# Kernel tuning notes

Measured on AMD Instinct MI355X. Metric: run time of the kernel, lower is better.

## Reference

```python
import jax, jax.numpy as jnp
import numpy as np

B, S, D, M = 8, 128, 512, 4
DEPTH, THR, TEMP, EPS = 16, 0.9999, 1.0, 1e-6


def setup_inputs() -> dict:
    key = jax.random.key(0)
    ks = jax.random.split(key, 13)
    def nrm(k, shape):
        return jax.random.normal(k, shape, jnp.float32) / np.sqrt(shape[-1]).astype(np.float32)
    return dict(
        x_real=jax.random.normal(ks[0], (B, S, D), jnp.float32),
        x_imag=jax.random.normal(ks[1], (B, S, D), jnp.float32),
        Wq_r=nrm(ks[2], (M, D, D)), Wq_i=nrm(ks[3], (M, D, D)),
        Wk_r=nrm(ks[4], (M, D, D)), Wk_i=nrm(ks[5], (M, D, D)),
        Wv_r=nrm(ks[6], (M, D, D)), Wv_i=nrm(ks[7], (M, D, D)),
        mod_bias=jnp.zeros((M, D), jnp.float32),
        ln_scale=jnp.ones((M, D), jnp.float32),
        ln_shift=jnp.zeros((M, D), jnp.float32),
        w_sal=nrm(ks[8], (M, 2 * D)),
        gru_Wih=nrm(ks[9], (2 * D, 3 * D)),
        gru_Whh=nrm(ks[10], (D, 3 * D)),
        gru_bih=jnp.zeros((3 * D,), jnp.float32),
        gru_bhh=jnp.zeros((3 * D,), jnp.float32),
        bias_W=nrm(ks[11], (D, M)),
        bias_b=jnp.zeros((M,), jnp.float32),
        w_halt=nrm(ks[12], (2 * D,)),
        b_halt=jnp.zeros((1,), jnp.float32),
    )


def reference(x_real, x_imag, Wq_r, Wq_i, Wk_r, Wk_i, Wv_r, Wv_i,
              mod_bias, ln_scale, ln_shift, w_sal,
              gru_Wih, gru_Whh, gru_bih, gru_bhh,
              bias_W, bias_b, w_halt, b_halt):
    scale = D ** -0.5

    def clin(xr, xi, Wr, Wi):
        # ComplexLinear broadcast over module axis: x [B,S,D], W [M,D,D] -> [M,B,S,D]
        rr = jnp.einsum('bsd,mde->mbse', xr, Wr)
        ii = jnp.einsum('bsd,mde->mbse', xi, Wi)
        ri = jnp.einsum('bsd,mde->mbse', xr, Wi)
        ir = jnp.einsum('bsd,mde->mbse', xi, Wr)
        return rr - ii, ri + ir

    def modules(zr, zi):
        # all M processor modules in parallel: ComplexAttention -> ModReLU -> ComplexLayerNorm
        qr, qi = clin(zr, zi, Wq_r, Wq_i)
        kr, ki = clin(zr, zi, Wk_r, Wk_i)
        vr, vi = clin(zr, zi, Wv_r, Wv_i)
        qf = jnp.concatenate([qr, qi], -1)            # [M,B,S,2D]
        kf = jnp.concatenate([kr, ki], -1)
        attn = jax.nn.softmax(jnp.einsum('mbsd,mbtd->mbst', qf, kf) * scale, -1)
        or_ = jnp.einsum('mbst,mbtd->mbsd', attn, vr)
        oi_ = jnp.einsum('mbst,mbtd->mbsd', attn, vi)
        # ModReLU
        mag = jnp.sqrt(or_ ** 2 + oi_ ** 2) + EPS
        g = jax.nn.relu(mag + mod_bias[:, None, None, :]) / mag
        or_, oi_ = or_ * g, oi_ * g
        # ComplexLayerNorm (normalize magnitude, keep phase; torch var is unbiased)
        mag = jnp.sqrt(or_ ** 2 + oi_ ** 2) + EPS
        mu = mag.mean(-1, keepdims=True)
        var = jnp.var(mag, axis=-1, keepdims=True, ddof=1)
        nm = (mag - mu) / jnp.sqrt(var + EPS)
        nm = nm * ln_scale[:, None, None, :] + ln_shift[:, None, None, :]
        ph = jnp.arctan2(oi_, or_)
        return nm * jnp.cos(ph), nm * jnp.sin(ph)

    def gru(xf, h):
        gx = xf @ gru_Wih + gru_bih
        gh = h @ gru_Whh + gru_bhh
        xr_, xz_, xn_ = jnp.split(gx, 3, -1)
        hr_, hz_, hn_ = jnp.split(gh, 3, -1)
        r = jax.nn.sigmoid(xr_ + hr_)
        zg = jax.nn.sigmoid(xz_ + hz_)
        n = jnp.tanh(xn_ + r * hn_)
        return (1.0 - zg) * n + zg * h

    def step(carry, _):
        zr, zi, h, cum, ar, ai, pond = carry
        pooled = jnp.concatenate([zr.mean(1), zi.mean(1)], -1)   # [B,2D]
        h = gru(pooled, h)                                       # ExecutiveController
        mbias = h @ bias_W + bias_b                              # [B,M]
        mr, mi = modules(zr, zi)                                 # [M,B,S,D]
        feat = jnp.concatenate([mr.mean(2), mi.mean(2)], -1)     # [M,B,2D]
        sal = jnp.einsum('mbf,mf->mb', feat, w_sal)              # salience
        w = jax.nn.softmax((sal + mbias.T) / TEMP, axis=0)       # module competition
        gr = jnp.einsum('mb,mbsd->bsd', w, mr)                   # global workspace broadcast
        gi = jnp.einsum('mb,mbsd->bsd', w, mi)
        gwp = jnp.concatenate([gr.mean(1), gi.mean(1)], -1)
        p = jax.nn.sigmoid(gwp @ w_halt + b_halt[0])             # [B] halting prob
        still = (cum < THR).astype(p.dtype)
        new_halt = ((cum + p) >= THR) & (cum < THR)
        wt = jnp.where(new_halt, 1.0 - cum, p) * still           # ACT weights
        cum = cum + wt
        ar = ar + wt[:, None, None] * gr
        ai = ai + wt[:, None, None] * gi
        pond = pond + still
        return (gr, gi, h, cum, ar, ai, pond), None

    z0 = jnp.zeros((B,), x_real.dtype)
    init = (x_real, x_imag, jnp.zeros((B, D), x_real.dtype), z0,
            jnp.zeros_like(x_real), jnp.zeros_like(x_imag), z0)
    (zr, zi, h, cum, ar, ai, pond), _ = jax.lax.scan(step, init, None, length=DEPTH)
    return jnp.stack([ar, ai])  # [2,B,S,D] accumulated workspace (real, imag)
```

## Files before the change

kernel.cpp:

```cpp
#include <hip/hip_runtime.h>
#include <math.h>

#define B 8
#define S 128
#define D 512
#define M 4
#define BS 1024
#define BSD 524288
#define DEPTH 16
#define THRESH 0.9999f
#define EPS 1e-6f
#define SCALE 0.04419417382415922f

typedef float floatx4 __attribute__((ext_vector_type(4)));
typedef short s8v __attribute__((ext_vector_type(8)));
typedef unsigned short us4 __attribute__((ext_vector_type(4)));

__device__ __forceinline__ unsigned short f2bf(float f) {
  unsigned int u = __float_as_uint(f);
  u += 0x7FFFu + ((u >> 16) & 1u);
  return (unsigned short)(u >> 16);
}
__device__ __forceinline__ float bf2f(unsigned short h) {
  return __uint_as_float((unsigned int)h << 16);
}

__device__ __forceinline__ void gll16(const void* g, void* l) {
  __builtin_amdgcn_global_load_lds(
      (const __attribute__((address_space(1))) unsigned int*)g,
      (__attribute__((address_space(3))) unsigned int*)l, 16, 0, 0);
}

#define OFF_ZR   0
#define OFF_ZI   (1*BSD)
#define OFF_AR   (2*BSD)
#define OFF_AI   (3*BSD)
#define OFF_OR   (4*BSD)
#define OFF_OI   (8*BSD)
#define OFF_FEAT (12*BSD)
#define OFF_GWP  (12*BSD + 65536)
#define OFF_H0   (12*BSD + 73728)
#define OFF_H1   (12*BSD + 77824)
#define OFF_CUM  (12*BSD + 81920)
#define OFF_W    (12*BSD + 81928)
#define OFF_WT   (12*BSD + 81960)
#define OFF_CUM2 (12*BSD + 81968)
#define OFF_PART OFF_ZR
#define OFF_XH   (12*BSD + 90112)
#define OFF_XL   (OFF_XH + 1*BSD)
#define OFF_WH   (OFF_XH + 2*BSD)
#define OFF_WL   (OFF_XH + 8*BSD)
#define OFF_QCH  (OFF_XH + 14*BSD)
#define OFF_QCL  (OFF_XH + 18*BSD)
#define OFF_KCH  (OFF_XH + 22*BSD)
#define OFF_KCL  (OFF_XH + 26*BSD)
#define OFF_VTH  (OFF_XH + 30*BSD)
#define OFF_VTL  (OFF_XH + 34*BSD)
#define OFF_PH   (OFF_XH + 38*BSD)
#define OFF_PL   (OFF_PH + 262144)

__global__ __launch_bounds__(256) void k_init(const float* __restrict__ xr,
                                              const float* __restrict__ xi,
                                              float* __restrict__ ws) {
  unsigned short* xh = (unsigned short*)(ws + OFF_XH);
  unsigned short* xl = (unsigned short*)(ws + OFF_XL);
  int i4 = blockIdx.x * 256 + threadIdx.x;
  float4 a = ((const float4*)xr)[i4];
  float4 b = ((const float4*)xi)[i4];
  ((float4*)(ws + OFF_ZR))[i4] = a;
  ((float4*)(ws + OFF_ZI))[i4] = b;
  float4 z = {0.f, 0.f, 0.f, 0.f};
  ((float4*)(ws + OFF_AR))[i4] = z;
  ((float4*)(ws + OFF_AI))[i4] = z;
  int row = i4 >> 7;
  int d4 = (i4 & 127) * 4;
  float av[4] = {a.x, a.y, a.z, a.w}, bv[4] = {b.x, b.y, b.z, b.w};
  us4 hh, hl;
#pragma unroll
  for (int j = 0; j < 4; ++j) {
    unsigned short h = f2bf(av[j]); hh[j] = h; hl[j] = f2bf(av[j] - bf2f(h));
  }
  *(us4*)(xh + (size_t)row * 1024 + d4) = hh;
  *(us4*)(xl + (size_t)row * 1024 + d4) = hl;
#pragma unroll
  for (int j = 0; j < 4; ++j) {
    unsigned short h = f2bf(bv[j]); hh[j] = h; hl[j] = f2bf(bv[j] - bf2f(h));
  }
  *(us4*)(xh + (size_t)row * 1024 + 512 + d4) = hh;
  *(us4*)(xl + (size_t)row * 1024 + 512 + d4) = hl;
  if (i4 < (B * D) / 4) {
    ((float4*)(ws + OFF_H0))[i4] = z;
    ((float4*)(ws + OFF_H1))[i4] = z;
  }
  if (i4 < 16384) ((float4*)(ws + OFF_FEAT))[i4] = z;
  if (i4 < 2048)  ((float4*)(ws + OFF_GWP))[i4] = z;
  if (i4 < B) { ws[OFF_CUM + i4] = 0.f; ws[OFF_CUM2 + i4] = 0.f; }
}

__global__ __launch_bounds__(256) void k_wprep(const float* __restrict__ Wqr,
                                               const float* __restrict__ Wqi,
                                               const float* __restrict__ Wkr,
                                               const float* __restrict__ Wki,
                                               const float* __restrict__ Wvr,
                                               const float* __restrict__ Wvi,
                                               float* __restrict__ ws) {
  __shared__ float lt[64][65];
  unsigned short* wh = (unsigned short*)(ws + OFF_WH);
  unsigned short* wl = (unsigned short*)(ws + OFF_WL);
  int z = blockIdx.z, m = z / 6, idx = z % 6;
  const float* Wsrc;
  switch (idx) {
    case 0:  Wsrc = Wqr; break;
    case 1:  Wsrc = Wqi; break;
    case 2:  Wsrc = Wkr; break;
    case 3:  Wsrc = Wki; break;
    case 4:  Wsrc = Wvr; break;
    default: Wsrc = Wvi; break;
  }
  Wsrc += (size_t)m * D * D;
  int k0 = blockIdx.x * 64, n0 = blockIdx.y * 64;
  int tx = threadIdx.x & 63, ty = threadIdx.x >> 6;
#pragma unroll
  for (int i = 0; i < 16; ++i) {
    int kl = ty + i * 4;
    lt[kl][tx] = Wsrc[(size_t)(k0 + kl) * D + n0 + tx];
  }
  __syncthreads();
  unsigned short* whp = wh + (size_t)z * 262144;
  unsigned short* wlp = wl + (size_t)z * 262144;
#pragma unroll
  for (int i = 0; i < 16; ++i) {
    int nl = ty + i * 4;
    float v = lt[tx][nl];
    unsigned short h = f2bf(v);
    whp[(size_t)(n0 + nl) * 512 + k0 + tx] = h;
    wlp[(size_t)(n0 + nl) * 512 + k0 + tx] = f2bf(v - bf2f(h));
  }
}

__global__ __launch_bounds__(256) void k_gwp(const float* __restrict__ zr,
                                             const float* __restrict__ zi,
                                             float* __restrict__ gwp) {
  int idx = blockIdx.x * 256 + threadIdx.x;
  int b = idx >> 10;
  int f = idx & 1023;
  const float* src = (f < D) ? (zr + b * S * D + f) : (zi + b * S * D + (f - D));
  float s = 0.f;
#pragma unroll 8
  for (int ss = 0; ss < S; ++ss) s += src[ss * D];
  gwp[idx] = s * (1.0f / S);
}

__global__ __launch_bounds__(256) void k_qk(float* __restrict__ ws) {
  __shared__ __align__(16) unsigned short Ah[128 * 32], Al[128 * 32];
  __shared__ __align__(16) unsigned short Bh[128 * 32], Bl[128 * 32];
  int t = threadIdx.x;
  if (blockIdx.x == 0 && blockIdx.y == 0 && blockIdx.z == 0) {
    float4 z4 = {0.f, 0.f, 0.f, 0.f};
    for (int i = t; i < 4096; i += 256) ((float4*)(ws + OFF_PART))[i] = z4;
  }
  const unsigned short* xh = (const unsigned short*)(ws + OFF_XH);
  const unsigned short* xl = (const unsigned short*)(ws + OFF_XL);
  const unsigned short* wh = (const unsigned short*)(ws + OFF_WH);
  const unsigned short* wl = (const unsigned short*)(ws + OFF_WL);
  int z = blockIdx.z, m = z >> 2, w6 = z & 3;
  int pair = (w6 >> 1) * 2;
  int p1 = m * 6 + pair + (w6 & 1);
  int p2 = m * 6 + pair + ((w6 & 1) ^ 1);
  bool neg2 = ((w6 & 1) == 0);
  const unsigned short* PH1 = wh + (size_t)p1 * 262144;
  const unsigned short* PL1 = wl + (size_t)p1 * 262144;
  const unsigned short* PH2 = wh + (size_t)p2 * 262144;
  const unsigned short* PL2 = wl + (size_t)p2 * 262144;

  int row0 = blockIdx.y * 128;
  int col0 = blockIdx.x * 128;
  int lane = t & 63, w = t >> 6;
  int wr = w >> 1, wc = w & 1;
  int q = lane >> 4, r = lane & 15;
  int srow = t >> 2;
  int skoff = (t & 3) * 8;
  size_t wrow1 = (size_t)(col0 + srow) * 512 + skoff;
  size_t wrow2 = (size_t)(col0 + 64 + srow) * 512 + skoff;
  size_t xrow1 = (size_t)(row0 + srow) * 1024 + skoff;
  size_t xrow2 = (size_t)(row0 + 64 + srow) * 1024 + skoff;
  const s8v sgn = {(short)0x8000, (short)0x8000, (short)0x8000, (short)0x8000,
                   (short)0x8000, (short)0x8000, (short)0x8000, (short)0x8000};

  floatx4 acc[4][4];
#pragma unroll
  for (int i = 0; i < 4; ++i)
#pragma unroll
    for (int j = 0; j < 4; ++j) acc[i][j] = (floatx4){0.f, 0.f, 0.f, 0.f};

  for (int k0 = 0; k0 < 1024; k0 += 32) {
    const unsigned short *WgH, *WgL;
    int kk = k0;
    bool xon = false;
    if (k0 < 512) { WgH = PH1; WgL = PL1; }
    else          { WgH = PH2; WgL = PL2; kk = k0 - 512; xon = neg2; }
    gll16(xh + xrow1 + k0, (char*)Ah + t * 16);
    gll16(xh + xrow2 + k0, (char*)Ah + 4096 + t * 16);
    gll16(xl + xrow1 + k0, (char*)Al + t * 16);
    gll16(xl + xrow2 + k0, (char*)Al + 4096 + t * 16);
    gll16(WgH + wrow1 + kk, (char*)Bh + t * 16);
    gll16(WgH + wrow2 + kk, (char*)Bh + 4096 + t * 16);
    gll16(WgL + wrow1 + kk, (char*)Bl + t * 16);
    gll16(WgL + wrow2 + kk, (char*)Bl + 4096 + t * 16);
    __syncthreads();
    s8v ah[4], al[4], bh[4], bl[4];
#pragma unroll
    for (int i = 0; i < 4; ++i) {
      int ro = (wr * 64 + i * 16 + r) * 32 + q * 8;
      ah[i] = *(const s8v*)((const short*)Ah + ro);
      al[i] = *(const s8v*)((const short*)Al + ro);
    }
#pragma unroll
    for (int j = 0; j < 4; ++j) {
      int ro = (wc * 64 + j * 16 + r) * 32 + q * 8;
      bh[j] = *(const s8v*)((const short*)Bh + ro);
      bl[j] = *(const s8v*)((const short*)Bl + ro);
    }
    if (xon) {
#pragma unroll
      for (int j = 0; j < 4; ++j) { bh[j] = bh[j] ^ sgn; bl[j] = bl[j] ^ sgn; }
    }
#pragma unroll
    for (int i = 0; i < 4; ++i)
#pragma unroll
      for (int j = 0; j < 4; ++j) {
        acc[i][j] = __builtin_amdgcn_mfma_f32_16x16x32_bf16(ah[i], bh[j], acc[i][j], 0, 0, 0);
        acc[i][j] = __builtin_amdgcn_mfma_f32_16x16x32_bf16(ah[i], bl[j], acc[i][j], 0, 0, 0);
        acc[i][j] = __builtin_amdgcn_mfma_f32_16x16x32_bf16(al[i], bh[j], acc[i][j], 0, 0, 0);
      }
    __syncthreads();
  }
  unsigned short *dh, *dl;
  if (w6 < 2) { dh = (unsigned short*)(ws + OFF_QCH); dl = (unsigned short*)(ws + OFF_QCL); }
  else        { dh = (unsigned short*)(ws + OFF_KCH); dl = (unsigned short*)(ws + OFF_KCL); }
  int half = (w6 & 1) * 512;
  size_t base = (size_t)m * 1024 * 1024;
#pragma unroll
  for (int i = 0; i < 4; ++i)
#pragma unroll
    for (int j = 0; j < 4; ++j) {
      int rowb = row0 + wr * 64 + i * 16 + q * 4;
      int colb = col0 + wc * 64 + j * 16 + r;
#pragma unroll
      for (int reg = 0; reg < 4; ++reg) {
        float v = acc[i][j][reg];
        unsigned short h = f2bf(v);
        size_t idx = base + (size_t)(rowb + reg) * 1024 + half + colb;
        dh[idx] = h;
        dl[idx] = f2bf(v - bf2f(h));
      }
    }
}

__global__ __launch_bounds__(256) void k_vattn(float* __restrict__ ws,
                                               const float* __restrict__ gwp,
                                               const float* __restrict__ hold,
                                               const float* __restrict__ Wih,
                                               const float* __restrict__ Whh) {
  __shared__ __align__(16) unsigned short Ah[128 * 32], Al[128 * 32];
  __shared__ __align__(16) unsigned short Bh[128 * 32], Bl[128 * 32];
  __shared__ float rmax[64][4];
  __shared__ float rsum[64][4];
  int t = threadIdx.x;
  int blk = blockIdx.x;

  if (blk >= 320) {
    float* xbuf = (float*)Ah;
    float* hbuf = (float*)Al;
    float (*red)[64][4] = (float (*)[64][4])Bh;
    int idx = blk - 320;
    int b = idx >> 5;
    int cc = (idx >> 2) & 7;
    int kq = idx & 3;
    int c0 = cc * 64;
    int td = t & 63, ks = t >> 6;
    for (int f = t; f < 1024; f += 256) xbuf[f] = gwp[b * 1024 + f];
    for (int d2 = t; d2 < 512; d2 += 256) hbuf[d2] = hold[b * 512 + d2];
    __syncthreads();
    float aR = 0.f, aZ = 0.f, aXn = 0.f, aHn = 0.f;
    int kbeg = kq * 384 + ks * 96, kend = kbeg + 96;
#pragma unroll 8
    for (int kk = kbeg; kk < kend; ++kk) {
      bool ih = kk < 1024;
      float x = ih ? xbuf[kk] : hbuf[kk - 1024];
      const float* base = ih ? (Wih + (size_t)kk * 1536) : (Whh + (size_t)(kk - 1024) * 1536);
      float wr = base[c0 + td];
      float wz = base[512 + c0 + td];
      float wn = base[1024 + c0 + td];
      aR += x * wr;
      aZ += x * wz;
      if (ih) aXn += x * wn; else aHn += x * wn;
    }
    red[ks][td][0] = aR;
    red[ks][td][1] = aZ;
    red[ks][td][2] = aXn;
    red[ks][td][3] = aHn;
    __syncthreads();
    if (t < 64) {
      float r_ = 0.f, z_ = 0.f, xn = 0.f, hn = 0.f;
#pragma unroll
      for (int s = 0; s < 4; ++s) {
        r_ += red[s][t][0]; z_ += red[s][t][1]; xn += red[s][t][2]; hn += red[s][t][3];
      }
      float* part = ws + OFF_PART + ((size_t)b * 512 + c0 + t) * 4;
      atomicAdd(part + 0, r_);
      atomicAdd(part + 1, z_);
      atomicAdd(part + 2, xn);
      atomicAdd(part + 3, hn);
    }
    return;
  }

  if (blk >= 256) {
    const unsigned short* qch = (const unsigned short*)(ws + OFF_QCH);
    const unsigned short* qcl = (const unsigned short*)(ws + OFF_QCL);
    const unsigned short* kch = (const unsigned short*)(ws + OFF_KCH);
    const unsigned short* kcl = (const unsigned short*)(ws + OFF_KCL);
    unsigned short* ph = (unsigned short*)(ws + OFF_PH);
    unsigned short* pl = (unsigned short*)(ws + OFF_PL);
    int ablk = blk - 256, mb = ablk >> 1, half = ablk & 1;
    size_t gbase = (size_t)mb * 128 * 1024;
    int lane = t & 63, wc = t >> 6;
    int q = lane >> 4, r = lane & 15;
    int srow = t >> 2;
    int skoff = (t & 3) * 8;
    size_t arow = gbase + (size_t)(half * 64 + srow) * 1024 + skoff;
    size_t brow1 = gbase + (size_t)srow * 1024 + skoff;
    size_t brow2 = gbase + (size_t)(64 + srow) * 1024 + skoff;

    floatx4 acc[4][2];
#pragma unroll
    for (int i = 0; i < 4; ++i)
#pragma unroll
      for (int j = 0; j < 2; ++j) acc[i][j] = (floatx4){0.f, 0.f, 0.f, 0.f};

    for (int k0 = 0; k0 < 1024; k0 += 32) {
      gll16(qch + arow + k0, (char*)Ah + t * 16);
      gll16(qcl + arow + k0, (char*)Al + t * 16);
      gll16(kch + brow1 + k0, (char*)Bh + t * 16);
      gll16(kch + brow2 + k0, (char*)Bh + 4096 + t * 16);
      gll16(kcl + brow1 + k0, (char*)Bl + t * 16);
      gll16(kcl + brow2 + k0, (char*)Bl + 4096 + t * 16);
      __syncthreads();
      s8v ah[4], al[4], bh[2], bl[2];
#pragma unroll
      for (int i = 0; i < 4; ++i) {
        int ro = (i * 16 + r) * 32 + q * 8;
        ah[i] = *(const s8v*)((const short*)Ah + ro);
        al[i] = *(const s8v*)((const short*)Al + ro);
      }
#pragma unroll
      for (int j = 0; j < 2; ++j) {
        int ro = (wc * 32 + j * 16 + r) * 32 + q * 8;
        bh[j] = *(const s8v*)((const short*)Bh + ro);
        bl[j] = *(const s8v*)((const short*)Bl + ro);
      }
#pragma unroll
      for (int i = 0; i < 4; ++i)
#pragma unroll
        for (int j = 0; j < 2; ++j) {
          acc[i][j] = __builtin_amdgcn_mfma_f32_16x16x32_bf16(ah[i], bh[j], acc[i][j], 0, 0, 0);
          acc[i][j] = __builtin_amdgcn_mfma_f32_16x16x32_bf16(ah[i], bl[j], acc[i][j], 0, 0, 0);
          acc[i][j] = __builtin_amdgcn_mfma_f32_16x16x32_bf16(al[i], bh[j], acc[i][j], 0, 0, 0);
        }
      __syncthreads();
    }
#pragma unroll
    for (int i = 0; i < 4; ++i)
#pragma unroll
      for (int j = 0; j < 2; ++j)
#pragma unroll
        for (int reg = 0; reg < 4; ++reg) acc[i][j][reg] *= SCALE;
#pragma unroll
    for (int i = 0; i < 4; ++i)
#pragma unroll
      for (int reg = 0; reg < 4; ++reg) {
        float mx = fmaxf(acc[i][0][reg], acc[i][1][reg]);
        for (int o = 1; o < 16; o <<= 1) mx = fmaxf(mx, __shfl_xor(mx, o));
        if (r == 0) rmax[i * 16 + q * 4 + reg][wc] = mx;
      }
    __syncthreads();
#pragma unroll
    for (int i = 0; i < 4; ++i)
#pragma unroll
      for (int reg = 0; reg < 4; ++reg) {
        int row = i * 16 + q * 4 + reg;
        float gmx = fmaxf(fmaxf(rmax[row][0], rmax[row][1]),
                          fmaxf(rmax[row][2], rmax[row][3]));
        float sm = 0.f;
#pragma unroll
        for (int j = 0; j < 2; ++j) {
          float e = __expf(acc[i][j][reg] - gmx);
          acc[i][j][reg] = e;
          sm += e;
        }
        for (int o = 1; o < 16; o <<= 1) sm += __shfl_xor(sm, o);
        if (r == 0) rsum[row][wc] = sm;
      }
    __syncthreads();
#pragma unroll
    for (int i = 0; i < 4; ++i)
#pragma unroll
      for (int reg = 0; reg < 4; ++reg) {
        int row = i * 16 + q * 4 + reg;
        float inv = 1.f / (rsum[row][0] + rsum[row][1] + rsum[row][2] + rsum[row][3]);
        size_t rb = (size_t)(mb * 128 + half * 64 + row) * 128;
#pragma unroll
        for (int j = 0; j < 2; ++j) {
          float p = acc[i][j][reg] * inv;
          unsigned short h = f2bf(p);
          size_t idx = rb + wc * 32 + j * 16 + r;
          ph[idx] = h;
          pl[idx] = f2bf(p - bf2f(h));
        }
      }
    return;
  }

  const unsigned short* xh = (const unsigned short*)(ws + OFF_XH);
  const unsigned short* xl = (const unsigned short*)(ws + OFF_XL);
  const unsigned short* wh = (const unsigned short*)(ws + OFF_WH);
  const unsigned short* wl = (const unsigned short*)(ws + OFF_WL);
  int plane = blk >> 5, m = plane >> 1, w6 = 4 + (plane & 1);
  int bx = (blk & 31) >> 3, by = blk & 7;
  int p1 = m * 6 + 4 + (w6 & 1);
  int p2 = m * 6 + 4 + ((w6 & 1) ^ 1);
  bool neg2 = ((w6 & 1) == 0);
  const unsigned short* PH1 = wh + (size_t)p1 * 262144;
  const unsigned short* PL1 = wl + (size_t)p1 * 262144;
  const unsigned short* PH2 = wh + (size_t)p2 * 262144;
  const unsigned short* PL2 = wl + (size_t)p2 * 262144;

  int row0 = bx * 128;
  int col0 = by * 128;
  int lane = t & 63, w = t >> 6;
  int wr = w >> 1, wc = w & 1;
  int q = lane >> 4, r = lane & 15;
  int srow = t >> 2;
  int skoff = (t & 3) * 8;
  size_t wrow1 = (size_t)(row0 + srow) * 512 + skoff;
  size_t wrow2 = (size_t)(row0 + 64 + srow) * 512 + skoff;
  size_t xrow1 = (size_t)(col0 + srow) * 1024 + skoff;
  size_t xrow2 = (size_t)(col0 + 64 + srow) * 1024 + skoff;
  const s8v sgn = {(short)0x8000, (short)0x8000, (short)0x8000, (short)0x8000,
                   (short)0x8000, (short)0x8000, (short)0x8000, (short)0x8000};

  floatx4 acc[4][4];
#pragma unroll
  for (int i = 0; i < 4; ++i)
#pragma unroll
    for (int j = 0; j < 4; ++j) acc[i][j] = (floatx4){0.f, 0.f, 0.f, 0.f};

  for (int k0 = 0; k0 < 1024; k0 += 32) {
    const unsigned short *WgH, *WgL;
    int kk = k0;
    bool xon = false;
    if (k0 < 512) { WgH = PH1; WgL = PL1; }
    else          { WgH = PH2; WgL = PL2; kk = k0 - 512; xon = neg2; }
    gll16(WgH + wrow1 + kk, (char*)Ah + t * 16);
    gll16(WgH + wrow2 + kk, (char*)Ah + 4096 + t * 16);
    gll16(WgL + wrow1 + kk, (char*)Al + t * 16);
    gll16(WgL + wrow2 + kk, (char*)Al + 4096 + t * 16);
    gll16(xh + xrow1 + k0, (char*)Bh + t * 16);
    gll16(xh + xrow2 + k0, (char*)Bh + 4096 + t * 16);
    gll16(xl + xrow1 + k0, (char*)Bl + t * 16);
    gll16(xl + xrow2 + k0, (char*)Bl + 4096 + t * 16);
    __syncthreads();
    s8v ah[4], al[4], bh[4], bl[4];
#pragma unroll
    for (int i = 0; i < 4; ++i) {
      int ro = (wr * 64 + i * 16 + r) * 32 + q * 8;
      ah[i] = *(const s8v*)((const short*)Ah + ro);
      al[i] = *(const s8v*)((const short*)Al + ro);
    }
#pragma unroll
    for (int j = 0; j < 4; ++j) {
      int ro = (wc * 64 + j * 16 + r) * 32 + q * 8;
      bh[j] = *(const s8v*)((const short*)Bh + ro);
      bl[j] = *(const s8v*)((const short*)Bl + ro);
    }
    if (xon) {
#pragma unroll
      for (int i = 0; i < 4; ++i) { ah[i] = ah[i] ^ sgn; al[i] = al[i] ^ sgn; }
    }
#pragma unroll
    for (int i = 0; i < 4; ++i)
#pragma unroll
      for (int j = 0; j < 4; ++j) {
        acc[i][j] = __builtin_amdgcn_mfma_f32_16x16x32_bf16(ah[i], bh[j], acc[i][j], 0, 0, 0);
        acc[i][j] = __builtin_amdgcn_mfma_f32_16x16x32_bf16(ah[i], bl[j], acc[i][j], 0, 0, 0);
        acc[i][j] = __builtin_amdgcn_mfma_f32_16x16x32_bf16(al[i], bh[j], acc[i][j], 0, 0, 0);
      }
    __syncthreads();
  }
  unsigned short* dh = (unsigned short*)(ws + OFF_VTH);
  unsigned short* dl = (unsigned short*)(ws + OFF_VTL);
  size_t base = (size_t)((w6 & 1) * 4 + m) * 512 * 1024;
#pragma unroll
  for (int i = 0; i < 4; ++i)
#pragma unroll
    for (int j = 0; j < 4; ++j) {
      int rowb = row0 + wr * 64 + i * 16 + q * 4;
      int colb = col0 + wc * 64 + j * 16 + r;
#pragma unroll
      for (int reg = 0; reg < 4; ++reg) {
        float v = acc[i][j][reg];
        unsigned short h = f2bf(v);
        size_t idx = base + (size_t)(rowb + reg) * 1024 + colb;
        dh[idx] = h;
        dl[idx] = f2bf(v - bf2f(h));
      }
    }
}

__global__ __launch_bounds__(256) void k_pv(float* __restrict__ ws) {
  __shared__ __align__(16) unsigned short Ph_[128 * 32], Pl_[128 * 32];
  __shared__ __align__(16) unsigned short VrH[128 * 32], VrL[128 * 32];
  __shared__ __align__(16) unsigned short ViH[128 * 32], ViL[128 * 32];
  const unsigned short* ph = (const unsigned short*)(ws + OFF_PH);
  const unsigned short* pl = (const unsigned short*)(ws + OFF_PL);
  const unsigned short* vth = (const unsigned short*)(ws + OFF_VTH);
  const unsigned short* vtl = (const unsigned short*)(ws + OFF_VTL);
  int mb = blockIdx.y, m = mb >> 3, b = mb & 7;
  int col0 = blockIdx.x * 128;
  int t = threadIdx.x, lane = t & 63, w = t >> 6;
  int wr = w >> 1, wc = w & 1;
  int q = lane >> 4, r = lane & 15;
  int srow = t >> 2;
  int skoff = (t & 3) * 8;
  size_t prow1 = (size_t)(mb * 128 + srow) * 128 + skoff;
  size_t prow2 = (size_t)(mb * 128 + 64 + srow) * 128 + skoff;
  size_t vbr1 = ((size_t)(m * 512) + col0 + srow) * 1024 + b * 128 + skoff;
  size_t vbr2 = ((size_t)(m * 512) + col0 + 64 + srow) * 1024 + b * 128 + skoff;
  size_t vplane_i = (size_t)4 * 512 * 1024;

  floatx4 accR[4][4], accI[4][4];
#pragma unroll
  for (int i = 0; i < 4; ++i)
#pragma unroll
    for (int j = 0; j < 4; ++j) {
      accR[i][j] = (floatx4){0.f, 0.f, 0.f, 0.f};
      accI[i][j] = (floatx4){0.f, 0.f, 0.f, 0.f};
    }

  for (int k0 = 0; k0 < 128; k0 += 32) {
    gll16(ph + prow1 + k0, (char*)Ph_ + t * 16);
    gll16(ph + prow2 + k0, (char*)Ph_ + 4096 + t * 16);
    gll16(pl + prow1 + k0, (char*)Pl_ + t * 16);
    gll16(pl + prow2 + k0, (char*)Pl_ + 4096 + t * 16);
    gll16(vth + vbr1 + k0, (char*)VrH + t * 16);
    gll16(vth + vbr2 + k0, (char*)VrH + 4096 + t * 16);
    gll16(vtl + vbr1 + k0, (char*)VrL + t * 16);
    gll16(vtl + vbr2 + k0, (char*)VrL + 4096 + t * 16);
    gll16(vth + vplane_i + vbr1 + k0, (char*)ViH + t * 16);
    gll16(vth + vplane_i + vbr2 + k0, (char*)ViH + 4096 + t * 16);
    gll16(vtl + vplane_i + vbr1 + k0, (char*)ViL + t * 16);
    gll16(vtl + vplane_i + vbr2 + k0, (char*)ViL + 4096 + t * 16);
    __syncthreads();
    s8v ah[4], al[4];
#pragma unroll
    for (int i = 0; i < 4; ++i) {
      int ro = (wr * 64 + i * 16 + r) * 32 + q * 8;
      ah[i] = *(const s8v*)((const short*)Ph_ + ro);
      al[i] = *(const s8v*)((const short*)Pl_ + ro);
    }
#pragma unroll
    for (int j = 0; j < 4; ++j) {
      int ro = (wc * 64 + j * 16 + r) * 32 + q * 8;
      s8v vrh = *(const s8v*)((const short*)VrH + ro);
      s8v vrl = *(const s8v*)((const short*)VrL + ro);
      s8v vih = *(const s8v*)((const short*)ViH + ro);
      s8v vil = *(const s8v*)((const short*)ViL + ro);
#pragma unroll
      for (int i = 0; i < 4; ++i) {
        accR[i][j] = __builtin_amdgcn_mfma_f32_16x16x32_bf16(ah[i], vrh, accR[i][j], 0, 0, 0);
        accR[i][j] = __builtin_amdgcn_mfma_f32_16x16x32_bf16(ah[i], vrl, accR[i][j], 0, 0, 0);
        accR[i][j] = __builtin_amdgcn_mfma_f32_16x16x32_bf16(al[i], vrh, accR[i][j], 0, 0, 0);
        accI[i][j] = __builtin_amdgcn_mfma_f32_16x16x32_bf16(ah[i], vih, accI[i][j], 0, 0, 0);
        accI[i][j] = __builtin_amdgcn_mfma_f32_16x16x32_bf16(ah[i], vil, accI[i][j], 0, 0, 0);
        accI[i][j] = __builtin_amdgcn_mfma_f32_16x16x32_bf16(al[i], vih, accI[i][j], 0, 0, 0);
      }
    }
    __syncthreads();
  }
  float* orp = ws + OFF_OR + (size_t)mb * 128 * 512;
  float* oip = ws + OFF_OI + (size_t)mb * 128 * 512;
#pragma unroll
  for (int i = 0; i < 4; ++i)
#pragma unroll
    for (int j = 0; j < 4; ++j) {
      int rowb = wr * 64 + i * 16 + q * 4;
      int colb = col0 + wc * 64 + j * 16 + r;
#pragma unroll
      for (int reg = 0; reg < 4; ++reg) {
        orp[(size_t)(rowb + reg) * 512 + colb] = accR[i][j][reg];
        oip[(size_t)(rowb + reg) * 512 + colb] = accI[i][j][reg];
      }
    }
}

__global__ __launch_bounds__(256) void k_modlnfeat(float* __restrict__ ws,
                                                   const float* __restrict__ mod_bias,
                                                   const float* __restrict__ ln_scale,
                                                   const float* __restrict__ ln_shift,
                                                   const float* __restrict__ hold,
                                                   float* __restrict__ hnew,
                                                   const float* __restrict__ bih,
                                                   const float* __restrict__ bhh) {
  int blk = blockIdx.x;
  int t = threadIdx.x;
  if (blk >= 128) {
    int b = blk - 128;
    for (int c = t; c < 512; c += 256) {
      const float* part = ws + OFF_PART + ((size_t)b * 512 + c) * 4;
      float r_ = part[0] + bih[c] + bhh[c];
      float z_ = part[1] + bih[512 + c] + bhh[512 + c];
      float xn = part[2] + bih[1024 + c];
      float hn = part[3] + bhh[1024 + c];
      float r = 1.f / (1.f + expf(-r_));
      float z = 1.f / (1.f + expf(-z_));
      float n = tanhf(xn + r * hn);
      hnew[b * 512 + c] = (1.f - z) * n + z * hold[b * 512 + c];
    }
    return;
  }
  int mb = blk >> 2, grp = blk & 3;
  int m = mb >> 3;
  int w = t >> 6, l = t & 63;
  int e0 = l * 8;
  float mb_[8], lsc[8], lsh[8];
  *(float4*)&mb_[0] = *(const float4*)(mod_bias + m * 512 + e0);
  *(float4*)&mb_[4] = *(const float4*)(mod_bias + m * 512 + e0 + 4);
  *(float4*)&lsc[0] = *(const float4*)(ln_scale + m * 512 + e0);
  *(float4*)&lsc[4] = *(const float4*)(ln_scale + m * 512 + e0 + 4);
  *(float4*)&lsh[0] = *(const float4*)(ln_shift + m * 512 + e0);
  *(float4*)&lsh[4] = *(const float4*)(ln_shift + m * 512 + e0 + 4);
  float featR[8] = {}, featI[8] = {};
  for (int it = 0; it < 8; ++it) {
    int s = grp * 32 + it * 4 + w;
    float* orp = ws + OFF_OR + ((size_t)mb * 128 + s) * 512 + e0;
    float* oip = ws + OFF_OI + ((size_t)mb * 128 + s) * 512 + e0;
    float orv[8], oiv[8], magv[8];
    *(float4*)&orv[0] = *(const float4*)orp;
    *(float4*)&orv[4] = *(const float4*)(orp + 4);
    *(float4*)&oiv[0] = *(const float4*)oip;
    *(float4*)&oiv[4] = *(const float4*)(oip + 4);
    float sum = 0.f, sumsq = 0.f;
#pragma unroll
    for (int j = 0; j < 8; ++j) {
      float o_r = orv[j], o_i = oiv[j];
      float mag = sqrtf(o_r * o_r + o_i * o_i) + EPS;
      float g = fmaxf(mag + mb_[j], 0.f) / mag;
      o_r *= g; o_i *= g;
      orv[j] = o_r; oiv[j] = o_i;
      float mag2 = sqrtf(o_r * o_r + o_i * o_i) + EPS;
      magv[j] = mag2;
      sum += mag2;
      sumsq += mag2 * mag2;
    }
    for (int o = 1; o < 64; o <<= 1) {
      sum += __shfl_xor(sum, o);
      sumsq += __shfl_xor(sumsq, o);
    }
    float mu = sum * (1.f / D);
    float var = (sumsq - (float)D * mu * mu) * (1.f / (D - 1));
    float inv = 1.f / sqrtf(var + EPS);
#pragma unroll
    for (int j = 0; j < 8; ++j) {
      float nm = (magv[j] - mu) * inv * lsc[j] + lsh[j];
      float hyp = magv[j] - EPS;
      float cp, sp;
      if (hyp > 0.f) { cp = orv[j] / hyp; sp = oiv[j] / hyp; }
      else           { cp = 1.f;          sp = 0.f; }
      orv[j] = nm * cp;
      oiv[j] = nm * sp;
      featR[j] += orv[j];
      featI[j] += oiv[j];
    }
    *(float4*)orp = *(float4*)&orv[0];
    *(float4*)(orp + 4) = *(float4*)&orv[4];
    *(float4*)oip = *(float4*)&oiv[0];
    *(float4*)(oip + 4) = *(float4*)&oiv[4];
  }
  float* fb = ws + OFF_FEAT + (size_t)mb * 1024;
#pragma unroll
  for (int j = 0; j < 8; ++j) {
    atomicAdd(fb + e0 + j, featR[j] * (1.0f / S));
    atomicAdd(fb + 512 + e0 + j, featI[j] * (1.0f / S));
  }
}

__global__ __launch_bounds__(256) void k_wsel(float* __restrict__ ws,
                                              const float* __restrict__ hnew,
                                              const float* __restrict__ bias_W,
                                              const float* __restrict__ bias_b,
                                              const float* __restrict__ w_sal) {
  __shared__ float mb_s[B][M];
  __shared__ float sal_s[M][B];
  int t = threadIdx.x;
  int p = t >> 3, l = t & 7;
  {
    int b = p >> 2, m = p & 3;
    float s = 0.f;
    for (int d2 = l; d2 < D; d2 += 8) s += hnew[b * D + d2] * bias_W[d2 * M + m];
    for (int o = 1; o < 8; o <<= 1) s += __shfl_xor(s, o);
    if (l == 0) mb_s[b][m] = s + bias_b[m];
  }
  {
    int m = p >> 3, b = p & 7;
    float s = 0.f;
    for (int f = l; f < 2 * D; f += 8) s += ws[OFF_FEAT + (m * B + b) * 2 * D + f] * w_sal[m * 2 * D + f];
    for (int o = 1; o < 8; o <<= 1) s += __shfl_xor(s, o);
    if (l == 0) sal_s[m][b] = s;
  }
  __syncthreads();
  if (t < B) {
    int b = t;
    float lg[M], mx = -1e30f;
#pragma unroll
    for (int m = 0; m < M; ++m) { lg[m] = sal_s[m][b] + mb_s[b][m]; mx = fmaxf(mx, lg[m]); }
    float sm = 0.f;
#pragma unroll
    for (int m = 0; m < M; ++m) { lg[m] = expf(lg[m] - mx); sm += lg[m]; }
    float inv = 1.f / sm;
#pragma unroll
    for (int m = 0; m < M; ++m) ws[OFF_W + m * B + b] = lg[m] * inv;
  }
  float4 z4 = {0.f, 0.f, 0.f, 0.f};
  for (int i = t; i < 16384; i += 256) ((float4*)(ws + OFF_FEAT))[i] = z4;
  for (int i = t; i < 2048; i += 256) ((float4*)(ws + OFF_GWP))[i] = z4;
}

__global__ __launch_bounds__(256) void k_bcast(float* __restrict__ ws) {
  __shared__ float pr[1024];
  unsigned short* xh = (unsigned short*)(ws + OFF_XH);
  unsigned short* xl = (unsigned short*)(ws + OFF_XL);
  int t = threadIdx.x;
  int i4 = blockIdx.x * 256 + t;
  int b = i4 >> 14;
  int l = t & 127;
  float w0 = ws[OFF_W + 0 * B + b], w1 = ws[OFF_W + 1 * B + b];
  float w2 = ws[OFF_W + 2 * B + b], w3 = ws[OFF_W + 3 * B + b];
  const float4* mr = (const float4*)(ws + OFF_OR);
  const float4* mi = (const float4*)(ws + OFF_OI);
  const int MS = BSD / 4;
  int row = i4 >> 7;
  int d4 = (i4 & 127) * 4;
  float4 r0 = mr[i4], r1 = mr[i4 + MS], r2 = mr[i4 + 2 * MS], r3 = mr[i4 + 3 * MS];
  float gvR[4];
  gvR[0] = w0 * r0.x + w1 * r1.x + w2 * r2.x + w3 * r3.x;
  gvR[1] = w0 * r0.y + w1 * r1.y + w2 * r2.y + w3 * r3.y;
  gvR[2] = w0 * r0.z + w1 * r1.z + w2 * r2.z + w3 * r3.z;
  gvR[3] = w0 * r0.w + w1 * r1.w + w2 * r2.w + w3 * r3.w;
  ((float4*)(ws + OFF_ZR))[i4] = (float4){gvR[0], gvR[1], gvR[2], gvR[3]};
  us4 hh, hl;
#pragma unroll
  for (int j = 0; j < 4; ++j) {
    unsigned short h = f2bf(gvR[j]); hh[j] = h; hl[j] = f2bf(gvR[j] - bf2f(h));
  }
  *(us4*)(xh + (size_t)row * 1024 + d4) = hh;
  *(us4*)(xl + (size_t)row * 1024 + d4) = hl;
  float4 s0 = mi[i4], s1 = mi[i4 + MS], s2 = mi[i4 + 2 * MS], s3 = mi[i4 + 3 * MS];
  float gvI[4];
  gvI[0] = w0 * s0.x + w1 * s1.x + w2 * s2.x + w3 * s3.x;
  gvI[1] = w0 * s0.y + w1 * s1.y + w2 * s2.y + w3 * s3.y;
  gvI[2] = w0 * s0.z + w1 * s1.z + w2 * s2.z + w3 * s3.z;
  gvI[3] = w0 * s0.w + w1 * s1.w + w2 * s2.w + w3 * s3.w;
  ((float4*)(ws + OFF_ZI))[i4] = (float4){gvI[0], gvI[1], gvI[2], gvI[3]};
#pragma unroll
  for (int j = 0; j < 4; ++j) {
    unsigned short h = f2bf(gvI[j]); hh[j] = h; hl[j] = f2bf(gvI[j] - bf2f(h));
  }
  *(us4*)(xh + (size_t)row * 1024 + 512 + d4) = hh;
  *(us4*)(xl + (size_t)row * 1024 + 512 + d4) = hl;
  if (t < 128) {
#pragma unroll
    for (int j = 0; j < 4; ++j) { pr[l * 4 + j] = gvR[j]; pr[512 + l * 4 + j] = gvI[j]; }
  }
  __syncthreads();
  if (t >= 128) {
#pragma unroll
    for (int j = 0; j < 4; ++j) { pr[l * 4 + j] += gvR[j]; pr[512 + l * 4 + j] += gvI[j]; }
  }
  __syncthreads();
  for (int pp = t; pp < 1024; pp += 256)
    atomicAdd(ws + OFF_GWP + b * 1024 + pp, pr[pp] * (1.0f / S));
}

__global__ __launch_bounds__(256) void k_acchalt(float* __restrict__ ws,
                                                 const float* __restrict__ w_halt,
                                                 const float* __restrict__ b_halt,
                                                 const float* __restrict__ cumr,
                                                 float* __restrict__ cumw) {
  __shared__ float sred[4];
  int t = threadIdx.x;
  int i4 = blockIdx.x * 256 + t;
  int b = i4 >> 14;
  float4 g = *(const float4*)(ws + OFF_GWP + b * 1024 + t * 4);
  float4 wv = *(const float4*)(w_halt + t * 4);
  float s = g.x * wv.x + g.y * wv.y + g.z * wv.z + g.w * wv.w;
  for (int o = 1; o < 64; o <<= 1) s += __shfl_xor(s, o);
  if ((t & 63) == 0) sred[t >> 6] = s;
  __syncthreads();
  float tot = sred[0] + sred[1] + sred[2] + sred[3];
  float p = 1.f / (1.f + expf(-(tot + b_halt[0])));
  float cum = cumr[b];
  float still = (cum < THRESH) ? 1.f : 0.f;
  bool nh = ((cum + p) >= THRESH) && (cum < THRESH);
  float wt = (nh ? (1.f - cum) : p) * still;
  if (((blockIdx.x & 63) == 0) && t == 0) cumw[b] = cum + wt;
  float4 z = ((const float4*)(ws + OFF_ZR))[i4];
  float4 a = ((float4*)(ws + OFF_AR))[i4];
  a.x += wt * z.x; a.y += wt * z.y; a.z += wt * z.z; a.w += wt * z.w;
  ((float4*)(ws + OFF_AR))[i4] = a;
  z = ((const float4*)(ws + OFF_ZI))[i4];
  a = ((float4*)(ws + OFF_AI))[i4];
  a.x += wt * z.x; a.y += wt * z.y; a.z += wt * z.z; a.w += wt * z.w;
  ((float4*)(ws + OFF_AI))[i4] = a;
}

__global__ __launch_bounds__(256) void k_out(const float* __restrict__ ws,
                                             float* __restrict__ out) {
  int i4 = blockIdx.x * 256 + threadIdx.x;
  ((float4*)out)[i4] = ((const float4*)(ws + OFF_AR))[i4];
  ((float4*)out)[i4 + BSD / 4] = ((const float4*)(ws + OFF_AI))[i4];
}

extern "C" void kernel_launch(void* const* d_in, const int* in_sizes, int n_in,
                              void* d_out, int out_size, void* d_ws, size_t ws_size,
                              hipStream_t stream) {
  (void)in_sizes; (void)n_in; (void)out_size; (void)ws_size;
  const float* x_real  = (const float*)d_in[0];
  const float* x_imag  = (const float*)d_in[1];
  const float* Wq_r    = (const float*)d_in[2];
  const float* Wq_i    = (const float*)d_in[3];
  const float* Wk_r    = (const float*)d_in[4];
  const float* Wk_i    = (const float*)d_in[5];
  const float* Wv_r    = (const float*)d_in[6];
  const float* Wv_i    = (const float*)d_in[7];
  const float* mod_bias = (const float*)d_in[8];
  const float* ln_scale = (const float*)d_in[9];
  const float* ln_shift = (const float*)d_in[10];
  const float* w_sal   = (const float*)d_in[11];
  const float* gru_Wih = (const float*)d_in[12];
  const float* gru_Whh = (const float*)d_in[13];
  const float* gru_bih = (const float*)d_in[14];
  const float* gru_bhh = (const float*)d_in[15];
  const float* bias_W  = (const float*)d_in[16];
  const float* bias_b  = (const float*)d_in[17];
  const float* w_halt  = (const float*)d_in[18];
  const float* b_halt  = (const float*)d_in[19];
  float* ws = (float*)d_ws;
  float* out = (float*)d_out;

  k_wprep<<<dim3(8, 8, 24), 256, 0, stream>>>(Wq_r, Wq_i, Wk_r, Wk_i, Wv_r, Wv_i, ws);
  k_init<<<512, 256, 0, stream>>>(x_real, x_imag, ws);
  k_gwp<<<32, 256, 0, stream>>>(ws + OFF_ZR, ws + OFF_ZI, ws + OFF_GWP);
  for (int step = 0; step < DEPTH; ++step) {
    const float* hold = ws + ((step & 1) ? OFF_H1 : OFF_H0);
    float* hnew = ws + ((step & 1) ? OFF_H0 : OFF_H1);
    const float* cumr = ws + ((step & 1) ? OFF_CUM2 : OFF_CUM);
    float* cumw = ws + ((step & 1) ? OFF_CUM : OFF_CUM2);
    k_qk<<<dim3(4, 8, 16), 256, 0, stream>>>(ws);
    k_vattn<<<576, 256, 0, stream>>>(ws, ws + OFF_GWP, hold, gru_Wih, gru_Whh);
    k_pv<<<dim3(4, 32), 256, 0, stream>>>(ws);
    k_modlnfeat<<<136, 256, 0, stream>>>(ws, mod_bias, ln_scale, ln_shift,
                                         hold, hnew, gru_bih, gru_bhh);
    k_wsel<<<1, 256, 0, stream>>>(ws, hnew, bias_W, bias_b, w_sal);
    k_bcast<<<512, 256, 0, stream>>>(ws);
    k_acchalt<<<512, 256, 0, stream>>>(ws, w_halt, b_halt, cumr, cumw);
  }
  k_out<<<512, 256, 0, stream>>>(ws, out);
}
```

Before: 3.406 ms.

## Derive halting from module features, fuse ACT accumulation into broadcast, split PV rows

```diff
diff --git a/kernel.cpp b/kernel.cpp
--- a/kernel.cpp
+++ b/kernel.cpp
@@ -519,29 +519,29 @@
 }
 
 __global__ __launch_bounds__(256) void k_pv(float* __restrict__ ws) {
-  __shared__ __align__(16) unsigned short Ph_[128 * 32], Pl_[128 * 32];
+  __shared__ __align__(16) unsigned short Ph_[64 * 32], Pl_[64 * 32];
   __shared__ __align__(16) unsigned short VrH[128 * 32], VrL[128 * 32];
   __shared__ __align__(16) unsigned short ViH[128 * 32], ViL[128 * 32];
   const unsigned short* ph = (const unsigned short*)(ws + OFF_PH);
   const unsigned short* pl = (const unsigned short*)(ws + OFF_PL);
   const unsigned short* vth = (const unsigned short*)(ws + OFF_VTH);
   const unsigned short* vtl = (const unsigned short*)(ws + OFF_VTL);
-  int mb = blockIdx.y, m = mb >> 3, b = mb & 7;
+  int yb = blockIdx.y, mb = yb >> 1, half = yb & 1;
+  int m = mb >> 3, b = mb & 7;
   int col0 = blockIdx.x * 128;
   int t = threadIdx.x, lane = t & 63, w = t >> 6;
   int wr = w >> 1, wc = w & 1;
   int q = lane >> 4, r = lane & 15;
   int srow = t >> 2;
   int skoff = (t & 3) * 8;
-  size_t prow1 = (size_t)(mb * 128 + srow) * 128 + skoff;
-  size_t prow2 = (size_t)(mb * 128 + 64 + srow) * 128 + skoff;
+  size_t prow = (size_t)(mb * 128 + half * 64 + srow) * 128 + skoff;
   size_t vbr1 = ((size_t)(m * 512) + col0 + srow) * 1024 + b * 128 + skoff;
   size_t vbr2 = ((size_t)(m * 512) + col0 + 64 + srow) * 1024 + b * 128 + skoff;
   size_t vplane_i = (size_t)4 * 512 * 1024;
 
-  floatx4 accR[4][4], accI[4][4];
-#pragma unroll
-  for (int i = 0; i < 4; ++i)
+  floatx4 accR[2][4], accI[2][4];
+#pragma unroll
+  for (int i = 0; i < 2; ++i)
 #pragma unroll
     for (int j = 0; j < 4; ++j) {
       accR[i][j] = (floatx4){0.f, 0.f, 0.f, 0.f};
@@ -549,10 +549,8 @@
     }
 
   for (int k0 = 0; k0 < 128; k0 += 32) {
-    gll16(ph + prow1 + k0, (char*)Ph_ + t * 16);
-    gll16(ph + prow2 + k0, (char*)Ph_ + 4096 + t * 16);
-    gll16(pl + prow1 + k0, (char*)Pl_ + t * 16);
-    gll16(pl + prow2 + k0, (char*)Pl_ + 4096 + t * 16);
+    gll16(ph + prow + k0, (char*)Ph_ + t * 16);
+    gll16(pl + prow + k0, (char*)Pl_ + t * 16);
     gll16(vth + vbr1 + k0, (char*)VrH + t * 16);
     gll16(vth + vbr2 + k0, (char*)VrH + 4096 + t * 16);
     gll16(vtl + vbr1 + k0, (char*)VrL + t * 16);
@@ -562,10 +560,10 @@
     gll16(vtl + vplane_i + vbr1 + k0, (char*)ViL + t * 16);
     gll16(vtl + vplane_i + vbr2 + k0, (char*)ViL + 4096 + t * 16);
     __syncthreads();
-    s8v ah[4], al[4];
-#pragma unroll
-    for (int i = 0; i < 4; ++i) {
-      int ro = (wr * 64 + i * 16 + r) * 32 + q * 8;
+    s8v ah[2], al[2];
+#pragma unroll
+    for (int i = 0; i < 2; ++i) {
+      int ro = (wr * 32 + i * 16 + r) * 32 + q * 8;
       ah[i] = *(const s8v*)((const short*)Ph_ + ro);
       al[i] = *(const s8v*)((const short*)Pl_ + ro);
     }
@@ -577,7 +575,7 @@
       s8v vih = *(const s8v*)((const short*)ViH + ro);
       s8v vil = *(const s8v*)((const short*)ViL + ro);
 #pragma unroll
-      for (int i = 0; i < 4; ++i) {
+      for (int i = 0; i < 2; ++i) {
         accR[i][j] = __builtin_amdgcn_mfma_f32_16x16x32_bf16(ah[i], vrh, accR[i][j], 0, 0, 0);
         accR[i][j] = __builtin_amdgcn_mfma_f32_16x16x32_bf16(ah[i], vrl, accR[i][j], 0, 0, 0);
         accR[i][j] = __builtin_amdgcn_mfma_f32_16x16x32_bf16(al[i], vrh, accR[i][j], 0, 0, 0);
@@ -591,10 +589,10 @@
   float* orp = ws + OFF_OR + (size_t)mb * 128 * 512;
   float* oip = ws + OFF_OI + (size_t)mb * 128 * 512;
 #pragma unroll
-  for (int i = 0; i < 4; ++i)
+  for (int i = 0; i < 2; ++i)
 #pragma unroll
     for (int j = 0; j < 4; ++j) {
-      int rowb = wr * 64 + i * 16 + q * 4;
+      int rowb = half * 64 + wr * 32 + i * 16 + q * 4;
       int colb = col0 + wc * 64 + j * 16 + r;
 #pragma unroll
       for (int reg = 0; reg < 4; ++reg) {
@@ -699,9 +697,15 @@
                                               const float* __restrict__ hnew,
                                               const float* __restrict__ bias_W,
                                               const float* __restrict__ bias_b,
-                                              const float* __restrict__ w_sal) {
+                                              const float* __restrict__ w_sal,
+                                              const float* __restrict__ w_halt,
+                                              const float* __restrict__ b_halt,
+                                              const float* __restrict__ cumr,
+                                              float* __restrict__ cumw) {
   __shared__ float mb_s[B][M];
   __shared__ float sal_s[M][B];
+  __shared__ float hsal_s[M][B];
+  __shared__ float wsm[M][B];
   int t = threadIdx.x;
   int p = t >> 3, l = t & 7;
   {
@@ -713,10 +717,14 @@
   }
   {
     int m = p >> 3, b = p & 7;
-    float s = 0.f;
-    for (int f = l; f < 2 * D; f += 8) s += ws[OFF_FEAT + (m * B + b) * 2 * D + f] * w_sal[m * 2 * D + f];
-    for (int o = 1; o < 8; o <<= 1) s += __shfl_xor(s, o);
-    if (l == 0) sal_s[m][b] = s;
+    float s = 0.f, s2 = 0.f;
+    for (int f = l; f < 2 * D; f += 8) {
+      float fv = ws[OFF_FEAT + (m * B + b) * 2 * D + f];
+      s += fv * w_sal[m * 2 * D + f];
+      s2 += fv * w_halt[f];
+    }
+    for (int o = 1; o < 8; o <<= 1) { s += __shfl_xor(s, o); s2 += __shfl_xor(s2, o); }
+    if (l == 0) { sal_s[m][b] = s; hsal_s[m][b] = s2; }
   }
   __syncthreads();
   if (t < B) {
@@ -728,24 +736,45 @@
 #pragma unroll
     for (int m = 0; m < M; ++m) { lg[m] = expf(lg[m] - mx); sm += lg[m]; }
     float inv = 1.f / sm;
-#pragma unroll
-    for (int m = 0; m < M; ++m) ws[OFF_W + m * B + b] = lg[m] * inv;
-  }
-  float4 z4 = {0.f, 0.f, 0.f, 0.f};
-  for (int i = t; i < 16384; i += 256) ((float4*)(ws + OFF_FEAT))[i] = z4;
-  for (int i = t; i < 2048; i += 256) ((float4*)(ws + OFF_GWP))[i] = z4;
+    float hs = 0.f;
+#pragma unroll
+    for (int m = 0; m < M; ++m) {
+      float wv = lg[m] * inv;
+      wsm[m][b] = wv;
+      ws[OFF_W + m * B + b] = wv;
+      hs += wv * hsal_s[m][b];
+    }
+    float pp = 1.f / (1.f + expf(-(hs + b_halt[0])));
+    float cum = cumr[b];
+    float still = (cum < THRESH) ? 1.f : 0.f;
+    bool nh = ((cum + pp) >= THRESH) && (cum < THRESH);
+    float wt = (nh ? (1.f - cum) : pp) * still;
+    cumw[b] = cum + wt;
+    ws[OFF_WT + b] = wt;
+  }
+  __syncthreads();
+  for (int idx = t; idx < 8192; idx += 256) {
+    int b = idx >> 10, f = idx & 1023;
+    float g = 0.f;
+#pragma unroll
+    for (int m = 0; m < M; ++m) {
+      size_t fi = OFF_FEAT + (size_t)(m * B + b) * 1024 + f;
+      g += wsm[m][b] * ws[fi];
+      ws[fi] = 0.f;
+    }
+    ws[OFF_GWP + idx] = g;
+  }
 }
 
 __global__ __launch_bounds__(256) void k_bcast(float* __restrict__ ws) {
-  __shared__ float pr[1024];
   unsigned short* xh = (unsigned short*)(ws + OFF_XH);
   unsigned short* xl = (unsigned short*)(ws + OFF_XL);
   int t = threadIdx.x;
   int i4 = blockIdx.x * 256 + t;
   int b = i4 >> 14;
-  int l = t & 127;
   float w0 = ws[OFF_W + 0 * B + b], w1 = ws[OFF_W + 1 * B + b];
   float w2 = ws[OFF_W + 2 * B + b], w3 = ws[OFF_W + 3 * B + b];
+  float wt = ws[OFF_WT + b];
   const float4* mr = (const float4*)(ws + OFF_OR);
   const float4* mi = (const float4*)(ws + OFF_OI);
   const int MS = BSD / 4;
@@ -757,7 +786,6 @@
   gvR[1] = w0 * r0.y + w1 * r1.y + w2 * r2.y + w3 * r3.y;
   gvR[2] = w0 * r0.z + w1 * r1.z + w2 * r2.z + w3 * r3.z;
   gvR[3] = w0 * r0.w + w1 * r1.w + w2 * r2.w + w3 * r3.w;
-  ((float4*)(ws + OFF_ZR))[i4] = (float4){gvR[0], gvR[1], gvR[2], gvR[3]};
   us4 hh, hl;
 #pragma unroll
   for (int j = 0; j < 4; ++j) {
@@ -771,56 +799,17 @@
   gvI[1] = w0 * s0.y + w1 * s1.y + w2 * s2.y + w3 * s3.y;
   gvI[2] = w0 * s0.z + w1 * s1.z + w2 * s2.z + w3 * s3.z;
   gvI[3] = w0 * s0.w + w1 * s1.w + w2 * s2.w + w3 * s3.w;
-  ((float4*)(ws + OFF_ZI))[i4] = (float4){gvI[0], gvI[1], gvI[2], gvI[3]};
 #pragma unroll
   for (int j = 0; j < 4; ++j) {
     unsigned short h = f2bf(gvI[j]); hh[j] = h; hl[j] = f2bf(gvI[j] - bf2f(h));
   }
   *(us4*)(xh + (size_t)row * 1024 + 512 + d4) = hh;
   *(us4*)(xl + (size_t)row * 1024 + 512 + d4) = hl;
-  if (t < 128) {
-#pragma unroll
-    for (int j = 0; j < 4; ++j) { pr[l * 4 + j] = gvR[j]; pr[512 + l * 4 + j] = gvI[j]; }
-  }
-  __syncthreads();
-  if (t >= 128) {
-#pragma unroll
-    for (int j = 0; j < 4; ++j) { pr[l * 4 + j] += gvR[j]; pr[512 + l * 4 + j] += gvI[j]; }
-  }
-  __syncthreads();
-  for (int pp = t; pp < 1024; pp += 256)
-    atomicAdd(ws + OFF_GWP + b * 1024 + pp, pr[pp] * (1.0f / S));
-}
-
-__global__ __launch_bounds__(256) void k_acchalt(float* __restrict__ ws,
-                                                 const float* __restrict__ w_halt,
-                                                 const float* __restrict__ b_halt,
-                                                 const float* __restrict__ cumr,
-                                                 float* __restrict__ cumw) {
-  __shared__ float sred[4];
-  int t = threadIdx.x;
-  int i4 = blockIdx.x * 256 + t;
-  int b = i4 >> 14;
-  float4 g = *(const float4*)(ws + OFF_GWP + b * 1024 + t * 4);
-  float4 wv = *(const float4*)(w_halt + t * 4);
-  float s = g.x * wv.x + g.y * wv.y + g.z * wv.z + g.w * wv.w;
-  for (int o = 1; o < 64; o <<= 1) s += __shfl_xor(s, o);
-  if ((t & 63) == 0) sred[t >> 6] = s;
-  __syncthreads();
-  float tot = sred[0] + sred[1] + sred[2] + sred[3];
-  float p = 1.f / (1.f + expf(-(tot + b_halt[0])));
-  float cum = cumr[b];
-  float still = (cum < THRESH) ? 1.f : 0.f;
-  bool nh = ((cum + p) >= THRESH) && (cum < THRESH);
-  float wt = (nh ? (1.f - cum) : p) * still;
-  if (((blockIdx.x & 63) == 0) && t == 0) cumw[b] = cum + wt;
-  float4 z = ((const float4*)(ws + OFF_ZR))[i4];
   float4 a = ((float4*)(ws + OFF_AR))[i4];
-  a.x += wt * z.x; a.y += wt * z.y; a.z += wt * z.z; a.w += wt * z.w;
+  a.x += wt * gvR[0]; a.y += wt * gvR[1]; a.z += wt * gvR[2]; a.w += wt * gvR[3];
   ((float4*)(ws + OFF_AR))[i4] = a;
-  z = ((const float4*)(ws + OFF_ZI))[i4];
   a = ((float4*)(ws + OFF_AI))[i4];
-  a.x += wt * z.x; a.y += wt * z.y; a.z += wt * z.z; a.w += wt * z.w;
+  a.x += wt * gvI[0]; a.y += wt * gvI[1]; a.z += wt * gvI[2]; a.w += wt * gvI[3];
   ((float4*)(ws + OFF_AI))[i4] = a;
 }
 
@@ -868,12 +857,12 @@
     float* cumw = ws + ((step & 1) ? OFF_CUM : OFF_CUM2);
     k_qk<<<dim3(4, 8, 16), 256, 0, stream>>>(ws);
     k_vattn<<<576, 256, 0, stream>>>(ws, ws + OFF_GWP, hold, gru_Wih, gru_Whh);
-    k_pv<<<dim3(4, 32), 256, 0, stream>>>(ws);
+    k_pv<<<dim3(4, 64), 256, 0, stream>>>(ws);
     k_modlnfeat<<<136, 256, 0, stream>>>(ws, mod_bias, ln_scale, ln_shift,
                                          hold, hnew, gru_bih, gru_bhh);
-    k_wsel<<<1, 256, 0, stream>>>(ws, hnew, bias_W, bias_b, w_sal);
+    k_wsel<<<1, 256, 0, stream>>>(ws, hnew, bias_W, bias_b, w_sal,
+                                  w_halt, b_halt, cumr, cumw);
     k_bcast<<<512, 256, 0, stream>>>(ws);
-    k_acchalt<<<512, 256, 0, stream>>>(ws, w_halt, b_halt, cumr, cumw);
   }
   k_out<<<512, 256, 0, stream>>>(ws, out);
 }
```

New measurement: 3.296 ms. 3.2% less time.
